# Kernel tuning notes

Hardware: AMD Instinct MI355X
Metric: run time of the kernel (lower is better)

## Reference

```python
import jax, jax.numpy as jnp
import numpy as np

DIM_V = 768
DIM_T = 768
HIDDEN = 256
MAX_KEEP = 96


def setup_inputs() -> dict:
    key = jax.random.key(0)
    k1, k2, k3, k4, k5 = jax.random.split(key, 5)
    B, N, S = 64, 1024, 64
    dense_visual = jax.random.normal(k1, (B, N, DIM_V), dtype=jnp.float32)
    text_embedding = jax.random.normal(k2, (B, S, DIM_T), dtype=jnp.float32)
    din = DIM_V + DIM_T
    # Linear params (stored as [in, out] for x @ W)
    W1 = jax.random.normal(k3, (din, HIDDEN), dtype=jnp.float32) / np.sqrt(din)
    b1 = jnp.zeros((HIDDEN,), dtype=jnp.float32)
    W2 = jax.random.normal(k4, (HIDDEN, 1), dtype=jnp.float32) / np.sqrt(HIDDEN)
    b2 = jnp.zeros((1,), dtype=jnp.float32)
    register_token = jax.random.normal(k5, (1, 1, DIM_V), dtype=jnp.float32) * 0.02
    return {
        "dense_visual": dense_visual,
        "text_embedding": text_embedding,
        "W1": W1, "b1": b1, "W2": W2, "b2": b2,
        "register_token": register_token,
    }


def reference(dense_visual, text_embedding, W1, b1, W2, b2, register_token):
    B, N, D = dense_visual.shape
    # Top-down context: mean-pooled text broadcast over patches
    ctx = jnp.broadcast_to(text_embedding.mean(axis=1, keepdims=True), (B, N, text_embedding.shape[-1]))
    scorer_in = jnp.concatenate([dense_visual, ctx], axis=-1)  # [B, N, 1536]
    h = jax.nn.relu(jnp.einsum('bnd,dh->bnh', scorer_in, W1) + b1)
    scores = jax.nn.sigmoid(jnp.einsum('bnh,ho->bno', h, W2) + b2).squeeze(-1)  # [B, N]
    num_keep = max(1, min(MAX_KEEP, N))
    _, top_k_idx = jax.lax.top_k(scores, num_keep)  # [B, K]
    top_k_idx = jnp.sort(top_k_idx, axis=1)
    sparse_visual = jnp.take_along_axis(dense_visual, top_k_idx[..., None], axis=1)  # [B, K, D]
    register = jnp.broadcast_to(register_token, (B, 1, D))
    final_visual = jnp.concatenate([sparse_visual, register], axis=1)  # [B, K+1, D]
    return final_visual, top_k_idx
```

## Files before the change

kernel.cpp:

```cpp
#include <hip/hip_runtime.h>
#include <hip/hip_bf16.h>

#define B_   64
#define N_   1024
#define S_   64
#define DV   768
#define DT   768
#define HID  256
#define KEEP 96

#define NKS (DV / 32)
#define SCALE_A 32.0f
#define SCALE_W 32.0f
#define SCALE_LOGIT (SCALE_A * SCALE_W)

typedef _Float16 half8_t __attribute__((ext_vector_type(8)));
typedef float f32x4 __attribute__((ext_vector_type(4)));

__global__ __launch_bounds__(256) void pack_w_kernel(
    const float* __restrict__ W1, _Float16* __restrict__ Wh,
    _Float16* __restrict__ Wl) {
  int d = blockIdx.x;
  int h = threadIdx.x;
  float w = W1[d * HID + h] * SCALE_W;
  _Float16 hi = (_Float16)w;
  _Float16 lo = (_Float16)(w - (float)hi);
  int ks = d >> 5, r = d & 31;
  int lane = ((r >> 3) << 4) | (h & 15);
  int i = r & 7, c = h >> 4;
  size_t off = ((size_t)((ks * 16 + c) * 64 + lane)) * 8 + i;
  Wh[off] = hi;
  Wl[off] = lo;
}

__global__ __launch_bounds__(256) void ctx_proj_kernel(
    const float* __restrict__ text,
    const float* __restrict__ W1,
    const float* __restrict__ b1,
    float* __restrict__ ctx_proj) {
  int b = blockIdx.x;
  int t = threadIdx.x;
  __shared__ float ctx[DT];
  #pragma unroll
  for (int j = 0; j < DT / 256; ++j) {
    int d = t + j * 256;
    float acc = 0.f;
    const float* p = text + (size_t)b * S_ * DT + d;
    for (int s = 0; s < S_; ++s) acc += p[(size_t)s * DT];
    ctx[d] = acc * (1.0f / S_);
  }
  __syncthreads();
  const float* wcol = W1 + (size_t)DV * HID + t;
  float s0 = 0.f, s1 = 0.f, s2 = 0.f, s3 = 0.f;
  for (int d = 0; d < DT; d += 4) {
    s0 = fmaf(ctx[d + 0], wcol[(size_t)(d + 0) * HID], s0);
    s1 = fmaf(ctx[d + 1], wcol[(size_t)(d + 1) * HID], s1);
    s2 = fmaf(ctx[d + 2], wcol[(size_t)(d + 2) * HID], s2);
    s3 = fmaf(ctx[d + 3], wcol[(size_t)(d + 3) * HID], s3);
  }
  ctx_proj[b * HID + t] = SCALE_LOGIT * (b1[t] + ((s0 + s1) + (s2 + s3)));
}

__global__ __launch_bounds__(256, 2) void score_kernel(
    const float* __restrict__ A,
    const _Float16* __restrict__ WhP,
    const _Float16* __restrict__ WlP,
    const float* __restrict__ W2,
    const float* __restrict__ ctx_proj,
    float* __restrict__ logits) {
  __shared__ half8_t AhS[4 * 64];
  __shared__ half8_t AlS[4 * 64];
  __shared__ float red[64][4];

  const int t = threadIdx.x;
  const int lane = t & 63;
  const int w = t >> 6;
  const int r0 = blockIdx.x * 64;
  const int batch = r0 >> 10;

  const int arow = t >> 2;
  const int akq = (t & 3) * 8;
  const float* aptr = A + (size_t)(r0 + arow) * DV + akq;
  const int adst = ((arow >> 4) * 64) + ((t & 3) << 4) + (arow & 15);

  const half8_t* WhV = (const half8_t*)WhP;
  const half8_t* WlV = (const half8_t*)WlP;

  f32x4 acc[4][4];
  #pragma unroll
  for (int rt = 0; rt < 4; ++rt)
    #pragma unroll
    for (int j = 0; j < 4; ++j) acc[rt][j] = (f32x4){0.f, 0.f, 0.f, 0.f};

  float4 a0 = *(const float4*)aptr;
  float4 a1 = *(const float4*)(aptr + 4);
  half8_t bh[2][4], bl[2][4];
  #pragma unroll
  for (int j = 0; j < 4; ++j) {
    int bi = (w * 4 + j) * 64 + lane;
    bh[0][j] = WhV[bi];
    bl[0][j] = WlV[bi];
  }

  #pragma unroll 2
  for (int ks = 0; ks < NKS; ++ks) {
    const int cur = ks & 1, nxt = cur ^ 1;
    half8_t hi8, lo8;
    {
      float av[8] = {a0.x, a0.y, a0.z, a0.w, a1.x, a1.y, a1.z, a1.w};
      #pragma unroll
      for (int i = 0; i < 8; ++i) {
        float x = av[i] * SCALE_A;
        _Float16 h = (_Float16)x;
        hi8[i] = h;
        lo8[i] = (_Float16)(x - (float)h);
      }
    }
    __syncthreads();
    AhS[adst] = hi8;
    AlS[adst] = lo8;
    __syncthreads();
    if (ks + 1 < NKS) {
      const float* ap = aptr + (ks + 1) * 32;
      a0 = *(const float4*)ap;
      a1 = *(const float4*)(ap + 4);
      #pragma unroll
      for (int j = 0; j < 4; ++j) {
        int bi = ((ks + 1) * 16 + w * 4 + j) * 64 + lane;
        bh[nxt][j] = WhV[bi];
        bl[nxt][j] = WlV[bi];
      }
    }
    half8_t ah[4], al[4];
    #pragma unroll
    for (int rt = 0; rt < 4; ++rt) {
      ah[rt] = AhS[rt * 64 + lane];
      al[rt] = AlS[rt * 64 + lane];
    }
    #pragma unroll
    for (int rt = 0; rt < 4; ++rt)
      #pragma unroll
      for (int j = 0; j < 4; ++j) {
        acc[rt][j] = __builtin_amdgcn_mfma_f32_16x16x32_f16(ah[rt], bh[cur][j], acc[rt][j], 0, 0, 0);
        acc[rt][j] = __builtin_amdgcn_mfma_f32_16x16x32_f16(ah[rt], bl[cur][j], acc[rt][j], 0, 0, 0);
        acc[rt][j] = __builtin_amdgcn_mfma_f32_16x16x32_f16(al[rt], bh[cur][j], acc[rt][j], 0, 0, 0);
      }
  }

  const int hbase = w * 64 + (lane & 15);
  const float* ctxp = ctx_proj + batch * HID;
  float psum[4][4];
  #pragma unroll
  for (int rt = 0; rt < 4; ++rt)
    #pragma unroll
    for (int r = 0; r < 4; ++r) psum[rt][r] = 0.f;
  #pragma unroll
  for (int j = 0; j < 4; ++j) {
    int hcol = hbase + j * 16;
    float cj = ctxp[hcol];
    float w2j = W2[hcol];
    #pragma unroll
    for (int rt = 0; rt < 4; ++rt)
      #pragma unroll
      for (int r = 0; r < 4; ++r)
        psum[rt][r] = fmaf(fmaxf(acc[rt][j][r] + cj, 0.f), w2j, psum[rt][r]);
  }
  #pragma unroll
  for (int m = 1; m < 16; m <<= 1)
    #pragma unroll
    for (int rt = 0; rt < 4; ++rt)
      #pragma unroll
      for (int r = 0; r < 4; ++r)
        psum[rt][r] += __shfl_xor(psum[rt][r], m, 64);
  if ((lane & 15) == 0) {
    int rowg = (lane >> 4) * 4;
    #pragma unroll
    for (int rt = 0; rt < 4; ++rt)
      #pragma unroll
      for (int r = 0; r < 4; ++r) red[rt * 16 + rowg + r][w] = psum[rt][r];
  }
  __syncthreads();
  if (t < 64) logits[r0 + t] = red[t][0] + red[t][1] + red[t][2] + red[t][3];
}

__global__ __launch_bounds__(1024) void topk_kernel(
    const float* __restrict__ logits,
    int* __restrict__ idx_ws,
    float* __restrict__ out,
    int out_idx_base) {
  int b = blockIdx.x;
  int t = threadIdx.x;
  __shared__ float s[N_];
  __shared__ int   si[N_];
  __shared__ int   t2[128];

  s[t]  = logits[b * N_ + t];
  si[t] = t;
  __syncthreads();

  for (int k = 2; k <= N_; k <<= 1) {
    for (int j = k >> 1; j > 0; j >>= 1) {
      int ixj = t ^ j;
      if (ixj > t) {
        float s1 = s[t], s2 = s[ixj];
        int   i1 = si[t], i2 = si[ixj];
        bool before = (s1 > s2) || (s1 == s2 && i1 < i2);
        bool doSwap = ((t & k) == 0) ? !before : before;
        if (doSwap) { s[t] = s2; s[ixj] = s1; si[t] = i2; si[ixj] = i1; }
      }
      __syncthreads();
    }
  }

  if (t < 128) t2[t] = (t < KEEP) ? si[t] : 0x7FFFFFFF;
  __syncthreads();
  for (int k = 2; k <= 128; k <<= 1) {
    for (int j = k >> 1; j > 0; j >>= 1) {
      if (t < 128) {
        int ixj = t ^ j;
        if (ixj > t) {
          int a = t2[t], c = t2[ixj];
          bool before = a < c;
          bool doSwap = ((t & k) == 0) ? !before : before;
          if (doSwap) { t2[t] = c; t2[ixj] = a; }
        }
      }
      __syncthreads();
    }
  }

  if (t < KEEP) {
    int v = t2[t];
    idx_ws[b * KEEP + t] = v;
    out[out_idx_base + b * KEEP + t] = (float)v;
  }
}

__global__ __launch_bounds__(192) void gather_kernel(
    const float* __restrict__ A,
    const float* __restrict__ reg_tok,
    const int* __restrict__ idx_ws,
    float* __restrict__ out) {
  int blk = blockIdx.x;
  int b = blk / (KEEP + 1), r = blk % (KEEP + 1);
  int t = threadIdx.x;
  const float* src;
  if (r == KEEP) {
    src = reg_tok;
  } else {
    int idx = idx_ws[b * KEEP + r];
    src = A + ((size_t)b * N_ + idx) * DV;
  }
  float4 v = *(const float4*)&src[t * 4];
  *(float4*)&out[((size_t)b * (KEEP + 1) + r) * DV + t * 4] = v;
}

extern "C" void kernel_launch(void* const* d_in, const int* in_sizes, int n_in,
                              void* d_out, int out_size, void* d_ws, size_t ws_size,
                              hipStream_t stream) {
  (void)in_sizes; (void)n_in; (void)out_size; (void)ws_size;
  const float* dense_visual = (const float*)d_in[0];
  const float* text_emb     = (const float*)d_in[1];
  const float* W1           = (const float*)d_in[2];
  const float* b1           = (const float*)d_in[3];
  const float* W2           = (const float*)d_in[4];
  const float* reg_tok      = (const float*)d_in[6];
  float* out = (float*)d_out;

  char* ws = (char*)d_ws;
  float*     ctx_proj = (float*)(ws + 0);
  float*     logits   = (float*)(ws + 65536);
  int*       idx_ws   = (int*)(ws + 327680);
  _Float16*  Wh       = (_Float16*)(ws + 352256);
  _Float16*  Wl       = (_Float16*)(ws + 745472);

  const int out_idx_base = B_ * (KEEP + 1) * DV;

  pack_w_kernel<<<DV, 256, 0, stream>>>(W1, Wh, Wl);
  ctx_proj_kernel<<<B_, 256, 0, stream>>>(text_emb, W1, b1, ctx_proj);
  score_kernel<<<(B_ * N_) / 64, 256, 0, stream>>>(dense_visual, Wh, Wl, W2, ctx_proj, logits);
  topk_kernel<<<B_, 1024, 0, stream>>>(logits, idx_ws, out, out_idx_base);
  gather_kernel<<<B_ * (KEEP + 1), 192, 0, stream>>>(dense_visual, reg_tok, idx_ws, out);
}
```

Before: 389.4 us.

## Double-buffer A tiles with 64-wide K steps and parallelize ctx projection

The score kernel now stages a 64-wide K slice of activations per iteration into double-buffered shared memory, cutting the barriers per iteration from two to one. The next slice's global loads are issued before the MFMA work and converted after it. Weight fragments are now loaded right before use instead of being register-prefetched one step ahead. The ctx projection kernel moves to 1024 threads, splitting the 768-long dot product into four partial sums reduced through shared memory, which adds parallelism to a small kernel.

New measurement: 378.7 us. -2.8%, faster.

```diff
diff --git a/kernel.cpp b/kernel.cpp
--- a/kernel.cpp
+++ b/kernel.cpp
@@ -9,7 +9,8 @@
 #define HID  256
 #define KEEP 96
 
-#define NKS (DV / 32)
+#define KB2  64
+#define NKS2 (DV / KB2)
 #define SCALE_A 32.0f
 #define SCALE_W 32.0f
 #define SCALE_LOGIT (SCALE_A * SCALE_W)
@@ -25,15 +26,15 @@
   float w = W1[d * HID + h] * SCALE_W;
   _Float16 hi = (_Float16)w;
   _Float16 lo = (_Float16)(w - (float)hi);
-  int ks = d >> 5, r = d & 31;
+  int g = d >> 5, r = d & 31;
   int lane = ((r >> 3) << 4) | (h & 15);
   int i = r & 7, c = h >> 4;
-  size_t off = ((size_t)((ks * 16 + c) * 64 + lane)) * 8 + i;
+  size_t off = ((size_t)((g * 16 + c) * 64 + lane)) * 8 + i;
   Wh[off] = hi;
   Wl[off] = lo;
 }
 
-__global__ __launch_bounds__(256) void ctx_proj_kernel(
+__global__ __launch_bounds__(1024) void ctx_proj_kernel(
     const float* __restrict__ text,
     const float* __restrict__ W1,
     const float* __restrict__ b1,
@@ -41,24 +42,47 @@
   int b = blockIdx.x;
   int t = threadIdx.x;
   __shared__ float ctx[DT];
-  #pragma unroll
-  for (int j = 0; j < DT / 256; ++j) {
-    int d = t + j * 256;
-    float acc = 0.f;
-    const float* p = text + (size_t)b * S_ * DT + d;
-    for (int s = 0; s < S_; ++s) acc += p[(size_t)s * DT];
-    ctx[d] = acc * (1.0f / S_);
-  }
-  __syncthreads();
-  const float* wcol = W1 + (size_t)DV * HID + t;
+  __shared__ float red[4][HID];
+  if (t < DT) {
+    const float* p = text + (size_t)b * S_ * DT + t;
+    float a0 = 0.f, a1 = 0.f, a2 = 0.f, a3 = 0.f;
+    for (int s = 0; s < S_; s += 4) {
+      a0 += p[(size_t)(s + 0) * DT];
+      a1 += p[(size_t)(s + 1) * DT];
+      a2 += p[(size_t)(s + 2) * DT];
+      a3 += p[(size_t)(s + 3) * DT];
+    }
+    ctx[t] = ((a0 + a1) + (a2 + a3)) * (1.0f / S_);
+  }
+  __syncthreads();
+  int p4 = t >> 8;
+  int h  = t & 255;
+  int db = p4 * 192;
+  const float* wcol = W1 + (size_t)(DV + db) * HID + h;
   float s0 = 0.f, s1 = 0.f, s2 = 0.f, s3 = 0.f;
-  for (int d = 0; d < DT; d += 4) {
-    s0 = fmaf(ctx[d + 0], wcol[(size_t)(d + 0) * HID], s0);
-    s1 = fmaf(ctx[d + 1], wcol[(size_t)(d + 1) * HID], s1);
-    s2 = fmaf(ctx[d + 2], wcol[(size_t)(d + 2) * HID], s2);
-    s3 = fmaf(ctx[d + 3], wcol[(size_t)(d + 3) * HID], s3);
-  }
-  ctx_proj[b * HID + t] = SCALE_LOGIT * (b1[t] + ((s0 + s1) + (s2 + s3)));
+  #pragma unroll 4
+  for (int d = 0; d < 192; d += 4) {
+    s0 = fmaf(ctx[db + d + 0], wcol[(size_t)(d + 0) * HID], s0);
+    s1 = fmaf(ctx[db + d + 1], wcol[(size_t)(d + 1) * HID], s1);
+    s2 = fmaf(ctx[db + d + 2], wcol[(size_t)(d + 2) * HID], s2);
+    s3 = fmaf(ctx[db + d + 3], wcol[(size_t)(d + 3) * HID], s3);
+  }
+  red[p4][h] = ((s0 + s1) + (s2 + s3));
+  __syncthreads();
+  if (t < HID)
+    ctx_proj[b * HID + t] =
+        SCALE_LOGIT * (b1[t] + ((red[0][t] + red[1][t]) + (red[2][t] + red[3][t])));
+}
+
+__device__ inline void cvt_split8(float4 a, float4 b, half8_t& hi, half8_t& lo) {
+  float x[8] = {a.x, a.y, a.z, a.w, b.x, b.y, b.z, b.w};
+  #pragma unroll
+  for (int i = 0; i < 8; ++i) {
+    float v = x[i] * SCALE_A;
+    _Float16 h = (_Float16)v;
+    hi[i] = h;
+    lo[i] = (_Float16)(v - (float)h);
+  }
 }
 
 __global__ __launch_bounds__(256, 2) void score_kernel(
@@ -68,8 +92,8 @@
     const float* __restrict__ W2,
     const float* __restrict__ ctx_proj,
     float* __restrict__ logits) {
-  __shared__ half8_t AhS[4 * 64];
-  __shared__ half8_t AlS[4 * 64];
+  __shared__ half8_t AhS[2][512];
+  __shared__ half8_t AlS[2][512];
   __shared__ float red[64][4];
 
   const int t = threadIdx.x;
@@ -79,9 +103,12 @@
   const int batch = r0 >> 10;
 
   const int arow = t >> 2;
-  const int akq = (t & 3) * 8;
-  const float* aptr = A + (size_t)(r0 + arow) * DV + akq;
-  const int adst = ((arow >> 4) * 64) + ((t & 3) << 4) + (arow & 15);
+  const int k0 = (t & 3) * 16;
+  const float* aptr = A + (size_t)(r0 + arow) * DV + k0;
+  const int ksub0 = k0 >> 5;
+  const int kq0 = (k0 & 31) >> 3;
+  const int dst1 = (ksub0 * 4 + kq0) * 64 + arow;
+  const int dst2 = dst1 + 64;
 
   const half8_t* WhV = (const half8_t*)WhP;
   const half8_t* WlV = (const half8_t*)WlP;
@@ -92,59 +119,63 @@
     #pragma unroll
     for (int j = 0; j < 4; ++j) acc[rt][j] = (f32x4){0.f, 0.f, 0.f, 0.f};
 
-  float4 a0 = *(const float4*)aptr;
-  float4 a1 = *(const float4*)(aptr + 4);
-  half8_t bh[2][4], bl[2][4];
-  #pragma unroll
-  for (int j = 0; j < 4; ++j) {
-    int bi = (w * 4 + j) * 64 + lane;
-    bh[0][j] = WhV[bi];
-    bl[0][j] = WlV[bi];
-  }
+  {
+    float4 v0 = *(const float4*)(aptr + 0);
+    float4 v1 = *(const float4*)(aptr + 4);
+    float4 v2 = *(const float4*)(aptr + 8);
+    float4 v3 = *(const float4*)(aptr + 12);
+    half8_t h0, l0, h1, l1;
+    cvt_split8(v0, v1, h0, l0);
+    cvt_split8(v2, v3, h1, l1);
+    AhS[0][dst1] = h0; AlS[0][dst1] = l0;
+    AhS[0][dst2] = h1; AlS[0][dst2] = l1;
+  }
+  __syncthreads();
 
   #pragma unroll 2
-  for (int ks = 0; ks < NKS; ++ks) {
-    const int cur = ks & 1, nxt = cur ^ 1;
-    half8_t hi8, lo8;
-    {
-      float av[8] = {a0.x, a0.y, a0.z, a0.w, a1.x, a1.y, a1.z, a1.w};
-      #pragma unroll
-      for (int i = 0; i < 8; ++i) {
-        float x = av[i] * SCALE_A;
-        _Float16 h = (_Float16)x;
-        hi8[i] = h;
-        lo8[i] = (_Float16)(x - (float)h);
+  for (int ks = 0; ks < NKS2; ++ks) {
+    const int cur = ks & 1;
+    float4 nv0, nv1, nv2, nv3;
+    if (ks + 1 < NKS2) {
+      const float* ap = aptr + (ks + 1) * KB2;
+      nv0 = *(const float4*)(ap + 0);
+      nv1 = *(const float4*)(ap + 4);
+      nv2 = *(const float4*)(ap + 8);
+      nv3 = *(const float4*)(ap + 12);
+    }
+    #pragma unroll
+    for (int ksub = 0; ksub < 2; ++ksub) {
+      half8_t bh[4], bl[4];
+      #pragma unroll
+      for (int j = 0; j < 4; ++j) {
+        int bi = ((ks * 2 + ksub) * 16 + w * 4 + j) * 64 + lane;
+        bh[j] = WhV[bi];
+        bl[j] = WlV[bi];
       }
+      half8_t ah[4], al[4];
+      #pragma unroll
+      for (int rt = 0; rt < 4; ++rt) {
+        int ai = (ksub * 4 + (lane >> 4)) * 64 + rt * 16 + (lane & 15);
+        ah[rt] = AhS[cur][ai];
+        al[rt] = AlS[cur][ai];
+      }
+      #pragma unroll
+      for (int rt = 0; rt < 4; ++rt)
+        #pragma unroll
+        for (int j = 0; j < 4; ++j) {
+          acc[rt][j] = __builtin_amdgcn_mfma_f32_16x16x32_f16(ah[rt], bh[j], acc[rt][j], 0, 0, 0);
+          acc[rt][j] = __builtin_amdgcn_mfma_f32_16x16x32_f16(ah[rt], bl[j], acc[rt][j], 0, 0, 0);
+          acc[rt][j] = __builtin_amdgcn_mfma_f32_16x16x32_f16(al[rt], bh[j], acc[rt][j], 0, 0, 0);
+        }
+    }
+    if (ks + 1 < NKS2) {
+      half8_t h0, l0, h1, l1;
+      cvt_split8(nv0, nv1, h0, l0);
+      cvt_split8(nv2, nv3, h1, l1);
+      AhS[cur ^ 1][dst1] = h0; AlS[cur ^ 1][dst1] = l0;
+      AhS[cur ^ 1][dst2] = h1; AlS[cur ^ 1][dst2] = l1;
     }
     __syncthreads();
-    AhS[adst] = hi8;
-    AlS[adst] = lo8;
-    __syncthreads();
-    if (ks + 1 < NKS) {
-      const float* ap = aptr + (ks + 1) * 32;
-      a0 = *(const float4*)ap;
-      a1 = *(const float4*)(ap + 4);
-      #pragma unroll
-      for (int j = 0; j < 4; ++j) {
-        int bi = ((ks + 1) * 16 + w * 4 + j) * 64 + lane;
-        bh[nxt][j] = WhV[bi];
-        bl[nxt][j] = WlV[bi];
-      }
-    }
-    half8_t ah[4], al[4];
-    #pragma unroll
-    for (int rt = 0; rt < 4; ++rt) {
-      ah[rt] = AhS[rt * 64 + lane];
-      al[rt] = AlS[rt * 64 + lane];
-    }
-    #pragma unroll
-    for (int rt = 0; rt < 4; ++rt)
-      #pragma unroll
-      for (int j = 0; j < 4; ++j) {
-        acc[rt][j] = __builtin_amdgcn_mfma_f32_16x16x32_f16(ah[rt], bh[cur][j], acc[rt][j], 0, 0, 0);
-        acc[rt][j] = __builtin_amdgcn_mfma_f32_16x16x32_f16(ah[rt], bl[cur][j], acc[rt][j], 0, 0, 0);
-        acc[rt][j] = __builtin_amdgcn_mfma_f32_16x16x32_f16(al[rt], bh[cur][j], acc[rt][j], 0, 0, 0);
-      }
   }
 
   const int hbase = w * 64 + (lane & 15);
@@ -277,7 +308,7 @@
   const int out_idx_base = B_ * (KEEP + 1) * DV;
 
   pack_w_kernel<<<DV, 256, 0, stream>>>(W1, Wh, Wl);
-  ctx_proj_kernel<<<B_, 256, 0, stream>>>(text_emb, W1, b1, ctx_proj);
+  ctx_proj_kernel<<<B_, 1024, 0, stream>>>(text_emb, W1, b1, ctx_proj);
   score_kernel<<<(B_ * N_) / 64, 256, 0, stream>>>(dense_visual, Wh, Wl, W2, ctx_proj, logits);
   topk_kernel<<<B_, 1024, 0, stream>>>(logits, idx_ws, out, out_idx_base);
   gather_kernel<<<B_ * (KEEP + 1), 192, 0, stream>>>(dense_visual, reg_tok, idx_ws, out);
```
